# Performance work log

Hardware: AMD Instinct MI355X
Metric: run time of the kernel (lower is better)

Reference implementation:

```python
import jax, jax.numpy as jnp
import numpy as np

N_BINS = 8
OUT = 224  # roi_align output_size hardcoded in the module


def _roi_align(flows, boxes):
    """torchvision-style roi_align, spatial_scale=1.0, aligned=False,
    one bilinear sample at each bin center (sampling_ratio=1).
    flows: (N, 2, H, W); boxes: (M, 5) -> (M, OUT, OUT, 2) channels-last."""
    N, C, H, W = flows.shape
    bidx = boxes[:, 0].astype(jnp.int32)
    x1, y1, x2, y2 = boxes[:, 1], boxes[:, 2], boxes[:, 3], boxes[:, 4]
    roi_w = jnp.maximum(x2 - x1, 1.0)
    roi_h = jnp.maximum(y2 - y1, 1.0)
    grid = (jnp.arange(OUT, dtype=flows.dtype) + 0.5) / OUT  # bin centers in [0,1)
    px = x1[:, None] + grid[None, :] * roi_w[:, None]  # (M, OUT)
    py = y1[:, None] + grid[None, :] * roi_h[:, None]  # (M, OUT)

    def axis(p, size):
        valid = (p >= -1.0) & (p <= size)
        pc = jnp.clip(p, 0.0, size - 1)
        lo = jnp.floor(pc).astype(jnp.int32)
        hi = jnp.minimum(lo + 1, size - 1)
        frac = pc - lo.astype(pc.dtype)
        return valid, lo, hi, frac

    vy, y0, y1i, fy = axis(py, H)
    vx, x0, x1i, fx = axis(px, W)

    b = bidx[:, None, None]  # broadcast to (M, OUT, OUT)

    def gather(yi, xi):
        # advanced indexing -> (M, OUT, OUT, C) channels-last
        return flows[b, :, yi[:, :, None], xi[:, None, :]]

    wy0 = (1 - fy)[:, :, None, None]
    wy1 = fy[:, :, None, None]
    wx0 = (1 - fx)[:, None, :, None]
    wx1 = fx[:, None, :, None]
    out = (gather(y0, x0) * wy0 * wx0 + gather(y0, x1i) * wy0 * wx1
           + gather(y1i, x0) * wy1 * wx0 + gather(y1i, x1i) * wy1 * wx1)
    mask = (vy[:, :, None] & vx[:, None, :])[..., None]
    return jnp.where(mask, out, 0.0)


def _velocity_histograms(flows, boxes):
    regions = _roi_align(flows, boxes)               # (M, OUT, OUT, 2)
    mag = jnp.sqrt(jnp.sum(regions * regions, -1))   # ||.||_2 over channel
    theta = jnp.arctan2(regions[..., 0], regions[..., 1])  # (M, OUT, OUT)
    M = boxes.shape[0]
    # uniform bins over [-pi, pi]; right edge inclusive (clip top bin)
    idx = jnp.floor((theta + jnp.pi) * (N_BINS / (2.0 * jnp.pi))).astype(jnp.int32)
    idx = jnp.clip(idx, 0, N_BINS - 1)
    seg = (jnp.arange(M, dtype=jnp.int32)[:, None] * N_BINS
           + idx.reshape(M, -1)).reshape(-1)
    flat_mag = mag.reshape(-1)
    sums = jax.ops.segment_sum(flat_mag, seg, num_segments=M * N_BINS)
    counts = jax.ops.segment_sum(jnp.ones_like(flat_mag), seg, num_segments=M * N_BINS)
    sums = sums.reshape(M, N_BINS)
    counts = counts.reshape(M, N_BINS)
    return jnp.where(counts != 0, sums / jnp.maximum(counts, 1.0), 0.0)


def setup_inputs() -> dict:
    key = jax.random.key(0)
    k1, k2, k3, k4, k5, k6 = jax.random.split(key, 6)
    N, H, W, M = 8, 512, 512, 512
    flows = jax.random.normal(k1, (N, 2, H, W), dtype=jnp.float32)
    b = jax.random.randint(k2, (M,), 0, N).astype(jnp.float32)
    x1 = jax.random.uniform(k3, (M,), minval=0.0, maxval=W - 256.0)
    y1 = jax.random.uniform(k4, (M,), minval=0.0, maxval=H - 256.0)
    bw = jax.random.uniform(k5, (M,), minval=32.0, maxval=224.0)
    bh = jax.random.uniform(k6, (M,), minval=32.0, maxval=224.0)
    boxes = jnp.stack([b, x1, y1, x1 + bw, y1 + bh], axis=1)
    return {"flows": flows, "boxes": boxes}


def reference(flows, boxes):
    return _velocity_histograms(flows, boxes)
```

## Files before the change

### kernel.cpp

```cpp
#include <hip/hip_runtime.h>
#include <math.h>

#define OUTSZ   224
#define NBINS   8
#define NTH     448
#define FNTH    256
#define IMG_H   512
#define IMG_W   512
#define HWSZ    (IMG_H * IMG_W)
#define SLOTS   512

typedef float f4u __attribute__((ext_vector_type(4), aligned(4)));

template <int CHUNKS>
__global__ __launch_bounds__(NTH) void velhist_kernel(
    const float* __restrict__ flows,
    const float* __restrict__ boxes,
    float* __restrict__ ws,
    float* __restrict__ out)
{
    constexpr int RPC = OUTSZ / CHUNKS;
    constexpr int RPT = RPC / 4;
    static_assert(RPC % 4 == 0, "4 row-streams need RPC % 4 == 0");
    const int bid   = blockIdx.x;
    const int m     = (CHUNKS == 1) ? bid : (bid / CHUNKS);
    const int chunk = (CHUNKS == 1) ? 0   : (bid - m * CHUNKS);
    const int tid   = threadIdx.x;

    __shared__ float s_h[2 * NBINS * SLOTS];

    for (int w = tid; w < 2 * NBINS * SLOTS; w += NTH)
        s_h[w] = 0.0f;

    const float bxf = boxes[m * 5 + 0];
    const float x1  = boxes[m * 5 + 1];
    const float y1  = boxes[m * 5 + 2];
    const float x2  = boxes[m * 5 + 3];
    const float y2  = boxes[m * 5 + 4];
    const int  bidx = (int)bxf;
    const float roi_w = fmaxf(x2 - x1, 1.0f);
    const float roi_h = fmaxf(y2 - y1, 1.0f);

    const float* __restrict__ f0 = flows + (size_t)bidx * 2 * HWSZ;
    const float* __restrict__ f1 = f0 + HWSZ;

    const float GINV = 1.0f / (float)OUTSZ;

    const int rq = tid / 112;
    const int cp = tid - rq * 112;
    const int c0 = cp << 1;

    const float px0 = x1 + ((float)c0 + 0.5f) * GINV * roi_w;
    const float px1 = x1 + ((float)c0 + 1.5f) * GINV * roi_w;
    const bool  vx0 = (px0 >= -1.0f) && (px0 <= (float)IMG_W);
    const bool  vx1 = (px1 >= -1.0f) && (px1 <= (float)IMG_W);
    const float pc0 = fminf(fmaxf(px0, 0.0f), (float)(IMG_W - 1));
    const float pc1 = fminf(fmaxf(px1, 0.0f), (float)(IMG_W - 1));
    const int   x00 = min((int)pc0, IMG_W - 2);
    const int   x01 = min((int)pc1, IMG_W - 2);
    const float fx0 = pc0 - (float)x00;
    const float fx1 = pc1 - (float)x01;
    const float wa0 = 1.0f - fx0, wa1 = fx0;
    const int   d   = min(x01 - x00, 2);
    const float wb0 = 1.0f - fx1, wb1 = fx1;
    const float g0 = (d == 0) ? wb0 : 0.0f;
    const float g1 = (d == 0) ? wb1 : ((d == 1) ? wb0 : 0.0f);
    const float g2 = (d == 1) ? wb1 : ((d == 2) ? wb0 : 0.0f);
    const float g3 = (d == 2) ? wb1 : 0.0f;
    const int   xb = x00;

    unsigned long long cnt_pk = 0ULL;

    __syncthreads();

    const int rowbase = chunk * RPC + rq * RPT;

    const bool interior = (x1 >= 0.0f) && (y1 >= 0.0f) &&
                          (x1 + roi_w <= (float)(IMG_W - 1)) &&
                          (y1 + roi_h <= (float)(IMG_H - 1));

    if (interior) {
        const float kdy = GINV * roi_h;
        const float py0 = fmaf((float)rowbase + 0.5f, kdy, y1);
        float i_f = 0.0f;
#pragma unroll 2
        for (int i = 0; i < RPT; ++i) {
            const float py = fmaf(i_f, kdy, py0);
            i_f += 1.0f;
            const int   y0 = (int)py;
            const float fy = py - (float)y0;
            const int   i0 = (y0 << 9) + xb;

            const f4u A0 = *reinterpret_cast<const f4u*>(f0 + i0);
            const f4u A1 = *reinterpret_cast<const f4u*>(f0 + i0 + IMG_W);
            const f4u B0 = *reinterpret_cast<const f4u*>(f1 + i0);
            const f4u B1 = *reinterpret_cast<const f4u*>(f1 + i0 + IMG_W);

            const float a0lo = A0.x * wa0 + A0.y * wa1;
            const float a0hi = A1.x * wa0 + A1.y * wa1;
            const float b0lo = B0.x * wa0 + B0.y * wa1;
            const float b0hi = B1.x * wa0 + B1.y * wa1;
            const float a0 = fmaf(fy, a0hi - a0lo, a0lo);
            const float b0 = fmaf(fy, b0hi - b0lo, b0lo);

            const float a1lo = A0.x * g0 + A0.y * g1 + A0.z * g2 + A0.w * g3;
            const float a1hi = A1.x * g0 + A1.y * g1 + A1.z * g2 + A1.w * g3;
            const float b1lo = B0.x * g0 + B0.y * g1 + B0.z * g2 + B0.w * g3;
            const float b1hi = B1.x * g0 + B1.y * g1 + B1.z * g2 + B1.w * g3;
            const float a1 = fmaf(fy, a1hi - a1lo, a1lo);
            const float b1 = fmaf(fy, b1hi - b1lo, b1lo);

            const float mag0 = __builtin_amdgcn_sqrtf(fmaf(a0, a0, b0 * b0));
            const float mag1 = __builtin_amdgcn_sqrtf(fmaf(a1, a1, b1 * b1));

            const unsigned au0 = __float_as_uint(a0), bu0 = __float_as_uint(b0);
            const unsigned na0 = au0 >> 31, nb0 = bu0 >> 31;
            const unsigned u0  = na0 ^ nb0;
            const unsigned t0  = ((au0 & 0x7fffffffu) >= (bu0 & 0x7fffffffu)) ? 1u : 0u;
            const int bin0 = (int)(((na0 ^ 1u) << 2) | (u0 << 1) | (u0 ^ t0));

            const unsigned au1 = __float_as_uint(a1), bu1 = __float_as_uint(b1);
            const unsigned na1 = au1 >> 31, nb1 = bu1 >> 31;
            const unsigned u1  = na1 ^ nb1;
            const unsigned t1  = ((au1 & 0x7fffffffu) >= (bu1 & 0x7fffffffu)) ? 1u : 0u;
            const int bin1 = (int)(((na1 ^ 1u) << 2) | (u1 << 1) | (u1 ^ t1));

            s_h[(bin0 << 9) + tid] += mag0;
            s_h[(bin1 << 9) + tid] += mag1;
            cnt_pk += (1ULL << (bin0 << 3)) + (1ULL << (bin1 << 3));
        }
    } else {
#pragma unroll 2
        for (int i = 0; i < RPT; ++i) {
            const int row = rowbase + i;
            const float gy  = ((float)row + 0.5f) * GINV;
            const float py  = y1 + gy * roi_h;
            const bool  vy  = (py >= -1.0f) && (py <= (float)IMG_H);
            const float pcy = fminf(fmaxf(py, 0.0f), (float)(IMG_H - 1));
            const int   y0  = min((int)pcy, IMG_H - 2);
            const float fy  = pcy - (float)y0;
            const float wy0 = 1.0f - fy;

            const int i0 = (y0 << 9) + xb;

            const f4u A0 = *reinterpret_cast<const f4u*>(f0 + i0);
            const f4u A1 = *reinterpret_cast<const f4u*>(f0 + i0 + IMG_W);
            const f4u B0 = *reinterpret_cast<const f4u*>(f1 + i0);
            const f4u B1 = *reinterpret_cast<const f4u*>(f1 + i0 + IMG_W);

            const float a0lo = A0.x * wa0 + A0.y * wa1;
            const float a0hi = A1.x * wa0 + A1.y * wa1;
            const float b0lo = B0.x * wa0 + B0.y * wa1;
            const float b0hi = B1.x * wa0 + B1.y * wa1;
            float a0 = wy0 * a0lo + fy * a0hi;
            float b0 = wy0 * b0lo + fy * b0hi;

            const float a1lo = A0.x * g0 + A0.y * g1 + A0.z * g2 + A0.w * g3;
            const float a1hi = A1.x * g0 + A1.y * g1 + A1.z * g2 + A1.w * g3;
            const float b1lo = B0.x * g0 + B0.y * g1 + B0.z * g2 + B0.w * g3;
            const float b1hi = B1.x * g0 + B1.y * g1 + B1.z * g2 + B1.w * g3;
            float a1 = wy0 * a1lo + fy * a1hi;
            float b1 = wy0 * b1lo + fy * b1hi;

            const bool valid0 = vx0 && vy;
            const bool valid1 = vx1 && vy;
            if (!valid0) { a0 = 0.0f; b0 = 0.0f; }
            if (!valid1) { a1 = 0.0f; b1 = 0.0f; }

            const float mag0 = __builtin_amdgcn_sqrtf(a0 * a0 + b0 * b0);
            const float mag1 = __builtin_amdgcn_sqrtf(a1 * a1 + b1 * b1);

            const int p0 = (a0 >= 0.0f) ? 1 : 0;
            const int q0 = (b0 >= 0.0f) ? 1 : 0;
            const int t0 = (fabsf(a0) >= fabsf(b0)) ? 1 : 0;
            const int u0 = p0 ^ q0;
            int bin0 = (p0 << 2) | (u0 << 1) | (u0 ^ t0);
            if (!valid0) bin0 = 4;

            const int p1 = (a1 >= 0.0f) ? 1 : 0;
            const int q1 = (b1 >= 0.0f) ? 1 : 0;
            const int t1 = (fabsf(a1) >= fabsf(b1)) ? 1 : 0;
            const int u1 = p1 ^ q1;
            int bin1 = (p1 << 2) | (u1 << 1) | (u1 ^ t1);
            if (!valid1) bin1 = 4;

            s_h[(bin0 << 9) + tid] += mag0;
            s_h[(bin1 << 9) + tid] += mag1;
            cnt_pk += (1ULL << (bin0 << 3)) + (1ULL << (bin1 << 3));
        }
    }

#pragma unroll
    for (int b = 0; b < NBINS; ++b)
        s_h[((NBINS + b) << 9) + tid] =
            (float)((unsigned)(cnt_pk >> (b << 3)) & 255u);

    int sh = 8;
    for (int off = 256; off >= 1; off >>= 1, --sh) {
        __syncthreads();
        for (int w = tid; w < 2 * NBINS * off; w += NTH) {
            const int b = w >> sh;
            const int t = w & (off - 1);
            s_h[(b << 9) + t] += s_h[(b << 9) + t + off];
        }
    }
    __syncthreads();

    if (tid < NBINS) {
        const float s = s_h[tid << 9];
        const float c = s_h[(NBINS + tid) << 9];
        if (CHUNKS == 1) {
            out[m * NBINS + tid] = (c != 0.0f) ? (s / fmaxf(c, 1.0f)) : 0.0f;
        } else {
            float* p = ws + bid * 16;
            p[tid]     = s;
            p[tid + 8] = c;
        }
    }
}

__global__ __launch_bounds__(FNTH) void finalize_kernel(
    const float* __restrict__ ws, float* __restrict__ out, int M, int chunks)
{
    const int i = blockIdx.x * FNTH + threadIdx.x;
    if (i >= M * NBINS) return;
    const int m = i >> 3;
    const int b = i & 7;
    float s = 0.0f, c = 0.0f;
    for (int ch = 0; ch < chunks; ++ch) {
        const float* p = ws + (size_t)(m * chunks + ch) * 16;
        s += p[b];
        c += p[b + 8];
    }
    out[i] = (c != 0.0f) ? (s / fmaxf(c, 1.0f)) : 0.0f;
}

extern "C" void kernel_launch(void* const* d_in, const int* in_sizes, int n_in,
                              void* d_out, int out_size, void* d_ws, size_t ws_size,
                              hipStream_t stream) {
    const float* flows = (const float*)d_in[0];
    const float* boxes = (const float*)d_in[1];
    float* out = (float*)d_out;
    const int M = in_sizes[1] / 5;

    const int CH = 4;
    const size_t part_need = (size_t)M * CH * 16 * sizeof(float);
    if (ws_size >= part_need) {
        velhist_kernel<CH><<<dim3(M * CH), dim3(NTH), 0, stream>>>(
            flows, boxes, (float*)d_ws, nullptr);
        finalize_kernel<<<dim3((M * NBINS + FNTH - 1) / FNTH), dim3(FNTH), 0, stream>>>(
            (const float*)d_ws, out, M, CH);
    } else {
        velhist_kernel<1><<<dim3(M), dim3(NTH), 0, stream>>>(
            flows, boxes, nullptr, out);
    }
}
```

Measured before the change: 103.0 us.

## Halve block size and replace LDS tree reduction with wavefront shuffle reduction

Shrinks the block from 448 to 256 threads (224 active), with each thread now covering twice as many output rows through 2 row-streams instead of 4. This halves the per-block LDS histogram. The multi-step LDS tree reduction with a barrier at every level is replaced by one pass in which each wave sums 4 slots per lane and then does a 64-lane shuffle reduction. The goal is to cut barrier and LDS traffic and allow more resident blocks. In exchange there is less thread-level parallelism per box and longer per-thread loops.

```diff
diff --git a/kernel.cpp b/kernel.cpp
--- a/kernel.cpp
+++ b/kernel.cpp
@@ -3,12 +3,13 @@
 
 #define OUTSZ   224
 #define NBINS   8
-#define NTH     448
+#define NTH     256
+#define ACT     224
 #define FNTH    256
 #define IMG_H   512
 #define IMG_W   512
 #define HWSZ    (IMG_H * IMG_W)
-#define SLOTS   512
+#define SLOTS   256
 
 typedef float f4u __attribute__((ext_vector_type(4), aligned(4)));
 
@@ -20,17 +21,19 @@
     float* __restrict__ out)
 {
     constexpr int RPC = OUTSZ / CHUNKS;
-    constexpr int RPT = RPC / 4;
-    static_assert(RPC % 4 == 0, "4 row-streams need RPC % 4 == 0");
+    constexpr int RPT = RPC / 2;
+    static_assert(RPC % 2 == 0, "2 row-streams need RPC % 2 == 0");
     const int bid   = blockIdx.x;
     const int m     = (CHUNKS == 1) ? bid : (bid / CHUNKS);
     const int chunk = (CHUNKS == 1) ? 0   : (bid - m * CHUNKS);
     const int tid   = threadIdx.x;
 
     __shared__ float s_h[2 * NBINS * SLOTS];
-
-    for (int w = tid; w < 2 * NBINS * SLOTS; w += NTH)
-        s_h[w] = 0.0f;
+    __shared__ float s_out[2 * NBINS];
+
+#pragma unroll
+    for (int b = 0; b < NBINS; ++b)
+        s_h[(b << 8) + tid] = 0.0f;
 
     const float bxf = boxes[m * 5 + 0];
     const float x1  = boxes[m * 5 + 1];
@@ -79,7 +82,8 @@
                           (x1 + roi_w <= (float)(IMG_W - 1)) &&
                           (y1 + roi_h <= (float)(IMG_H - 1));
 
-    if (interior) {
+    if (tid < ACT) {
+      if (interior) {
         const float kdy = GINV * roi_h;
         const float py0 = fmaf((float)rowbase + 0.5f, kdy, y1);
         float i_f = 0.0f;
@@ -125,11 +129,11 @@
             const unsigned t1  = ((au1 & 0x7fffffffu) >= (bu1 & 0x7fffffffu)) ? 1u : 0u;
             const int bin1 = (int)(((na1 ^ 1u) << 2) | (u1 << 1) | (u1 ^ t1));
 
-            s_h[(bin0 << 9) + tid] += mag0;
-            s_h[(bin1 << 9) + tid] += mag1;
+            s_h[(bin0 << 8) + tid] += mag0;
+            s_h[(bin1 << 8) + tid] += mag1;
             cnt_pk += (1ULL << (bin0 << 3)) + (1ULL << (bin1 << 3));
         }
-    } else {
+      } else {
 #pragma unroll 2
         for (int i = 0; i < RPT; ++i) {
             const int row = rowbase + i;
@@ -184,31 +188,41 @@
             int bin1 = (p1 << 2) | (u1 << 1) | (u1 ^ t1);
             if (!valid1) bin1 = 4;
 
-            s_h[(bin0 << 9) + tid] += mag0;
-            s_h[(bin1 << 9) + tid] += mag1;
+            s_h[(bin0 << 8) + tid] += mag0;
+            s_h[(bin1 << 8) + tid] += mag1;
             cnt_pk += (1ULL << (bin0 << 3)) + (1ULL << (bin1 << 3));
         }
+      }
     }
 
 #pragma unroll
     for (int b = 0; b < NBINS; ++b)
-        s_h[((NBINS + b) << 9) + tid] =
+        s_h[((NBINS + b) << 8) + tid] =
             (float)((unsigned)(cnt_pk >> (b << 3)) & 255u);
 
-    int sh = 8;
-    for (int off = 256; off >= 1; off >>= 1, --sh) {
-        __syncthreads();
-        for (int w = tid; w < 2 * NBINS * off; w += NTH) {
-            const int b = w >> sh;
-            const int t = w & (off - 1);
-            s_h[(b << 9) + t] += s_h[(b << 9) + t + off];
-        }
-    }
     __syncthreads();
 
+    {
+        const int lane = tid & 63;
+        const int wid  = tid >> 6;
+#pragma unroll
+        for (int k = 0; k < 4; ++k) {
+            const int b = (wid << 2) + k;
+            float v = s_h[(b << 8) + lane]
+                    + s_h[(b << 8) + lane + 64]
+                    + s_h[(b << 8) + lane + 128]
+                    + s_h[(b << 8) + lane + 192];
+#pragma unroll
+            for (int off = 32; off >= 1; off >>= 1)
+                v += __shfl_down(v, off, 64);
+            if (lane == 0) s_out[b] = v;
+        }
+    }
+    __syncthreads();
+
     if (tid < NBINS) {
-        const float s = s_h[tid << 9];
-        const float c = s_h[(NBINS + tid) << 9];
+        const float s = s_out[tid];
+        const float c = s_out[NBINS + tid];
         if (CHUNKS == 1) {
             out[m * NBINS + tid] = (c != 0.0f) ? (s / fmaxf(c, 1.0f)) : 0.0f;
         } else {
```

After: 97.37 us. 5.5% less time.
